# Kernel tuning notes

Hardware: AMD Instinct MI355X
Metric: run time of the kernel (lower is better)

## Reference

```python
import jax, jax.numpy as jnp
import numpy as np

GRID_SIZE = 5
SPLINE_ORDER = 3
FP_DIM = 2513        # mixed fingerprint: MACCS + PubChem + ErG + Morgan
FP_2_DIM = 512
HIDDEN_DIM = 300
BATCH = 8192


def make_grid(in_features):
    # Matches KANLinear buffer: arange(-so, gs+so+1)*h + grid_range[0], expanded per feature
    h = 2.0 / GRID_SIZE  # (grid_range[1]-grid_range[0]) / grid_size with range [-1, 1]
    g = jnp.arange(-SPLINE_ORDER, GRID_SIZE + SPLINE_ORDER + 1, dtype=jnp.float32) * h - 1.0
    return jnp.broadcast_to(g[None, :], (in_features, g.shape[0]))  # [in, 12]


def b_splines(x, grid):
    # x: [B, in] -> bases: [B, in, grid_size + spline_order]
    x = x[:, :, None]  # [B, in, 1]
    bases = ((x >= grid[:, :-1]) & (x < grid[:, 1:])).astype(x.dtype)
    for k in range(1, SPLINE_ORDER + 1):
        bases = ((x - grid[:, :-(k + 1)]) / (grid[:, k:-1] - grid[:, :-(k + 1)]) * bases[..., :-1]
                 + (grid[:, k + 1:] - x) / (grid[:, k + 1:] - grid[:, 1:-k]) * bases[..., 1:])
    return bases  # [B, in, K]


def kan_linear(x, base_w, spline_w, scaler):
    # base path: SiLU(x) @ base_w.T
    base_out = jax.nn.silu(x) @ base_w.T  # [B, out]
    # spline path: flatten bases and scaled spline weights into one GEMM
    in_f = x.shape[1]
    grid = make_grid(in_f)
    bs = b_splines(x, grid).reshape(x.shape[0], -1)               # [B, in*K]
    sw = (spline_w * scaler[:, :, None]).reshape(spline_w.shape[0], -1)  # [out, in*K]
    return base_out + bs @ sw.T


def setup_inputs() -> dict:
    key = jax.random.key(0)
    ks = jax.random.split(key, 8)
    K = GRID_SIZE + SPLINE_ORDER
    def kaiming(k, shape, fan_in):
        bound = 1.0 / np.sqrt(fan_in)
        return jax.random.uniform(k, shape, jnp.float32, -bound, bound)
    return {
        "fp": jax.random.uniform(ks[0], (BATCH, FP_DIM), jnp.float32),
        "base_w1": kaiming(ks[1], (FP_2_DIM, FP_DIM), FP_DIM),
        "spline_w1": jax.random.normal(ks[2], (FP_2_DIM, FP_DIM, K), jnp.float32) * 0.02,
        "scaler1": kaiming(ks[3], (FP_2_DIM, FP_DIM), FP_DIM),
        "base_w2": kaiming(ks[4], (HIDDEN_DIM, FP_2_DIM), FP_2_DIM),
        "spline_w2": jax.random.normal(ks[5], (HIDDEN_DIM, FP_2_DIM, K), jnp.float32) * 0.02,
        "scaler2": kaiming(ks[6], (HIDDEN_DIM, FP_2_DIM), FP_2_DIM),
    }


def reference(fp, base_w1, spline_w1, scaler1, base_w2, spline_w2, scaler2):
    # FPN forward (eval mode, dropout=identity): fc1 (KAN) -> ReLU -> fc2 (KAN)
    h = kan_linear(fp, base_w1, spline_w1, scaler1)   # [B, fp_2_dim]
    h = jax.nn.relu(h)
    out = kan_linear(h, base_w2, spline_w2, scaler2)  # [B, hidden]
    return out
```

## Files before the change

### kernel.cpp

```cpp
#include <hip/hip_runtime.h>
#include <stdint.h>

typedef unsigned short ushort_t;
typedef __attribute__((ext_vector_type(8))) __bf16 bf16x8;
typedef __attribute__((ext_vector_type(4))) float f32x4;
typedef __attribute__((ext_vector_type(4))) uint32_t u32x4;
typedef __attribute__((ext_vector_type(4))) float float4_t;

#define GPTR(x) ((__attribute__((address_space(1))) void*)(x))
#define LPTR(x) ((__attribute__((address_space(3))) void*)(x))

#define M8   8192
#define KT   5888
#define NKT  184
#define LDW1 17664
#define O1   512
#define K2   3584
#define NK2  112
#define O2P  384

__device__ __forceinline__ ushort_t f2b(float f) {
  union { float f; uint32_t i; } v; v.f = f;
  uint32_t x = v.i;
  uint32_t r = (x + 0x7FFFu + ((x >> 16) & 1u)) >> 16;
  return (ushort_t)r;
}

__device__ __forceinline__ void spline_expand(float x, float* sil, float* b ) {
  *sil = x / (1.0f + __expf(-x));
  float g[12];
#pragma unroll
  for (int j = 0; j < 12; ++j) g[j] = (float)(j - 3) * 0.4f - 1.0f;
  float t[11];
#pragma unroll
  for (int j = 0; j < 11; ++j) t[j] = (x >= g[j] && x < g[j + 1]) ? 1.0f : 0.0f;
#pragma unroll
  for (int k = 1; k <= 3; ++k) {
#pragma unroll
    for (int j = 0; j + k < 11; ++j) {
      float i1 = 1.0f / (g[j + k] - g[j]);
      float i2 = 1.0f / (g[j + k + 1] - g[j + 1]);
      t[j] = (x - g[j]) * i1 * t[j] + (g[j + k + 1] - x) * i2 * t[j + 1];
    }
  }
#pragma unroll
  for (int k = 0; k < 8; ++k) b[k] = t[k];
}

__global__ __launch_bounds__(256) void expand_third(
    const float* __restrict__ xin, ushort_t* __restrict__ A1t, int f0, int fcnt) {
  __shared__ __align__(16) ushort_t sb[KT];
  const int row = blockIdx.x, tid = threadIdx.x;
  for (int t = tid; t < (KT >> 1); t += 256) ((uint32_t*)sb)[t] = 0;
  __syncthreads();
  const float* xr = xin + (size_t)row * 2513 + f0;
#pragma unroll
  for (int j = 0; j < 1024; j += 256) {
    int fl = j + tid;
    if (fl < fcnt) {
      float sil, b[8];
      spline_expand(xr[fl], &sil, b);
      ushort_t* o = &sb[fl * 7];
      o[0] = f2b(sil);
#pragma unroll
      for (int k = 0; k < 6; ++k) o[1 + k] = f2b(b[2 + k]);
    }
  }
  __syncthreads();
  u32x4* dst = (u32x4*)(A1t + (size_t)row * KT);
  const u32x4* src = (const u32x4*)sb;
  for (int t = tid; t < (KT >> 3); t += 256) dst[t] = src[t];
}

__global__ __launch_bounds__(256) void prepw_all(
    const float* __restrict__ bw1, const float* __restrict__ sw1, const float* __restrict__ sc1,
    const float* __restrict__ bw2, const float* __restrict__ sw2, const float* __restrict__ sc2,
    ushort_t* __restrict__ W1, ushort_t* __restrict__ W2) {
  __shared__ __align__(16) ushort_t sb[KT];
  const int bx = blockIdx.x, c = blockIdx.y, tid = threadIdx.x;
  const float *bw, *sw, *sc;
  ushort_t* dst;
  int in_f, o, out_f, ce, f0, fcnt;
  if (bx < 512) {
    o = bx; out_f = 512; in_f = 2513;
    ce = KT; f0 = c * 838;
    fcnt = (c == 2) ? 837 : 838;
    dst = W1 + (size_t)o * LDW1 + c * KT;
    bw = bw1; sw = sw1; sc = sc1;
  } else {
    if (c > 0) return;
    o = bx - 512; out_f = 300; in_f = 512;
    ce = K2; f0 = 0; fcnt = 512;
    dst = W2 + (size_t)o * K2;
    bw = bw2; sw = sw2; sc = sc2;
  }
  for (int t = tid; t < (ce >> 1); t += 256) ((uint32_t*)sb)[t] = 0;
  __syncthreads();
  if (o < out_f) {
#pragma unroll
    for (int j = 0; j < 1024; j += 256) {
      int fl = j + tid;
      if (fl < fcnt) {
        size_t base = (size_t)o * in_f + f0 + fl;
        float s = sc[base];
        float4_t s0 = ((const float4_t*)(sw + base * 8))[0];
        float4_t s1 = ((const float4_t*)(sw + base * 8))[1];
        ushort_t* w = &sb[fl * 7];
        w[0] = f2b(bw[base]);
        w[1] = f2b(s0.z * s); w[2] = f2b(s0.w * s);
        w[3] = f2b(s1.x * s); w[4] = f2b(s1.y * s);
        w[5] = f2b(s1.z * s); w[6] = f2b(s1.w * s);
      }
    }
  }
  __syncthreads();
  u32x4* d4 = (u32x4*)dst;
  const u32x4* s4 = (const u32x4*)sb;
  for (int t = tid; t < (ce >> 3); t += 256) d4[t] = s4[t];
}


__global__ __launch_bounds__(256) void gemm1_kernel(
    const ushort_t* __restrict__ A, const ushort_t* __restrict__ Bw,
    float* __restrict__ P, int accum) {
  __shared__ __align__(16) ushort_t As[2][128 * 32];
  __shared__ __align__(16) ushort_t Bs[2][128 * 32];
  const int tid = threadIdx.x;
  const int m0 = blockIdx.x * 128;
  const int n0 = blockIdx.y * 128;
  const int s = blockIdx.z;
  const int k0 = s * 61;
  const int k1 = (s == 2) ? NKT : (k0 + 61);
  const int lane = tid & 63;
  const int wv = tid >> 6;
  const int wm = wv & 1, wn = wv >> 1;
  const int l15 = lane & 15, lq = lane >> 4;
  const int rxor = (l15 >> 2) & 1;
  const int csw = ((lq ^ (l15 & 3)) << 3);

  f32x4 acc[4][4];
#pragma unroll
  for (int a = 0; a < 4; ++a)
#pragma unroll
    for (int b = 0; b < 4; ++b) acc[a][b] = {0.0f, 0.0f, 0.0f, 0.0f};

  const int u0 = tid, u1 = tid + 256;
  const int r0 = u0 >> 2, c0 = u0 & 3;
  const int r1 = u1 >> 2, c1 = u1 & 3;
  const int lr0 = r0 ^ ((r0 >> 2) & 1), lc0 = c0 ^ (lr0 & 3);
  const int lr1 = r1 ^ ((r1 >> 2) & 1), lc1 = c1 ^ (lr1 & 3);
  const ushort_t* gA0 = A + (size_t)(m0 + lr0) * KT + lc0 * 8;
  const ushort_t* gA1 = A + (size_t)(m0 + lr1) * KT + lc1 * 8;
  const ushort_t* gB0 = Bw + (size_t)(n0 + lr0) * LDW1 + lc0 * 8;
  const ushort_t* gB1 = Bw + (size_t)(n0 + lr1) * LDW1 + lc1 * 8;

#define STG1(bb, kk) do { const int kb_ = (kk) << 5; \
    __builtin_amdgcn_global_load_lds(GPTR(gA0 + kb_), LPTR(&As[bb][u0 * 8]), 16, 0, 0); \
    __builtin_amdgcn_global_load_lds(GPTR(gA1 + kb_), LPTR(&As[bb][u1 * 8]), 16, 0, 0); \
    __builtin_amdgcn_global_load_lds(GPTR(gB0 + kb_), LPTR(&Bs[bb][u0 * 8]), 16, 0, 0); \
    __builtin_amdgcn_global_load_lds(GPTR(gB1 + kb_), LPTR(&Bs[bb][u1 * 8]), 16, 0, 0); \
  } while (0)

  STG1(0, k0);
  __syncthreads();
  const int nst = k1 - k0;
  for (int i = 0; i < nst; ++i) {
    const int cur = i & 1;
    if (i + 1 < nst) STG1(cur ^ 1, k0 + i + 1);
    bf16x8 aF[4], bF[4];
#pragma unroll
    for (int t = 0; t < 4; ++t) {
      const int ar = ((wm * 64 + t * 16 + l15) ^ rxor) * 32 + csw;
      const int br = ((wn * 64 + t * 16 + l15) ^ rxor) * 32 + csw;
      aF[t] = *(const bf16x8*)(&As[cur][ar]);
      bF[t] = *(const bf16x8*)(&Bs[cur][br]);
    }
#pragma unroll
    for (int ti = 0; ti < 4; ++ti)
#pragma unroll
      for (int tj = 0; tj < 4; ++tj)
        acc[ti][tj] = __builtin_amdgcn_mfma_f32_16x16x32_bf16(aF[ti], bF[tj], acc[ti][tj], 0, 0, 0);
    __syncthreads();
  }
#undef STG1

  float* Pp = P + (size_t)s * M8 * O1;
#pragma unroll
  for (int ti = 0; ti < 4; ++ti) {
#pragma unroll
    for (int tj = 0; tj < 4; ++tj) {
      int gr = m0 + wm * 64 + ti * 16 + lq * 4;
      int gc = n0 + wn * 64 + tj * 16 + l15;
#pragma unroll
      for (int rr = 0; rr < 4; ++rr) {
        size_t pi = (size_t)(gr + rr) * O1 + gc;
        float v = acc[ti][tj][rr];
        if (accum) v += Pp[pi];
        Pp[pi] = v;
      }
    }
  }
}

__global__ __launch_bounds__(256) void reduce_expand_stage(
    const float* __restrict__ P, ushort_t* __restrict__ A2) {
  __shared__ __align__(16) ushort_t sb[K2];
  const int row = blockIdx.x, tid = threadIdx.x;
  const size_t total = (size_t)M8 * O1;
#pragma unroll
  for (int j = 0; j < 512; j += 256) {
    int f = j + tid;
    size_t idx = (size_t)row * O1 + f;
    float v = P[idx] + P[total + idx] + P[2 * total + idx];
    if (v < 0.0f) v = 0.0f;
    float sil, b[8];
    spline_expand(v, &sil, b);
    ushort_t* o = &sb[f * 7];
    o[0] = f2b(sil);
#pragma unroll
    for (int k = 0; k < 6; ++k) o[1 + k] = f2b(b[2 + k]);
  }
  __syncthreads();
  u32x4* dst = (u32x4*)(A2 + (size_t)row * K2);
  const u32x4* src = (const u32x4*)sb;
  for (int t = tid; t < (K2 >> 3); t += 256) dst[t] = src[t];
}

__global__ __launch_bounds__(256) void gemm2_kernel(
    const ushort_t* __restrict__ A, const ushort_t* __restrict__ Bw,
    float* __restrict__ P2) {
  __shared__ __align__(16) ushort_t As[2][64 * 32];
  __shared__ __align__(16) ushort_t Bs[2][128 * 32];
  const int tid = threadIdx.x;
  const int m0 = blockIdx.x * 64;
  const int n0 = blockIdx.y * 128;
  const int s = blockIdx.z;
  const int k0 = s * 56, k1 = k0 + 56;
  const int lane = tid & 63;
  const int wv = tid >> 6;
  const int wm = wv & 1, wn = wv >> 1;
  const int l15 = lane & 15, lq = lane >> 4;
  const int rxor = (l15 >> 2) & 1;
  const int csw = ((lq ^ (l15 & 3)) << 3);

  f32x4 acc[2][4];
#pragma unroll
  for (int a = 0; a < 2; ++a)
#pragma unroll
    for (int b = 0; b < 4; ++b) acc[a][b] = {0.0f, 0.0f, 0.0f, 0.0f};

  const int uA = tid;
  const int rA = uA >> 2, cA = uA & 3;
  const int lrA = rA ^ ((rA >> 2) & 1), lcA = cA ^ (lrA & 3);
  const int u0 = tid, u1 = tid + 256;
  const int rB0 = u0 >> 2, cB0 = u0 & 3;
  const int rB1 = u1 >> 2, cB1 = u1 & 3;
  const int lrB0 = rB0 ^ ((rB0 >> 2) & 1), lcB0 = cB0 ^ (lrB0 & 3);
  const int lrB1 = rB1 ^ ((rB1 >> 2) & 1), lcB1 = cB1 ^ (lrB1 & 3);
  const ushort_t* gA  = A + (size_t)(m0 + lrA) * K2 + lcA * 8;
  const ushort_t* gB0 = Bw + (size_t)(n0 + lrB0) * K2 + lcB0 * 8;
  const ushort_t* gB1 = Bw + (size_t)(n0 + lrB1) * K2 + lcB1 * 8;

#define STG2(bb, kk) do { const int kb_ = (kk) << 5; \
    __builtin_amdgcn_global_load_lds(GPTR(gA + kb_),  LPTR(&As[bb][uA * 8]), 16, 0, 0); \
    __builtin_amdgcn_global_load_lds(GPTR(gB0 + kb_), LPTR(&Bs[bb][u0 * 8]), 16, 0, 0); \
    __builtin_amdgcn_global_load_lds(GPTR(gB1 + kb_), LPTR(&Bs[bb][u1 * 8]), 16, 0, 0); \
  } while (0)

  STG2(0, k0);
  __syncthreads();
  const int nst = k1 - k0;
  for (int i = 0; i < nst; ++i) {
    const int cur = i & 1;
    if (i + 1 < nst) STG2(cur ^ 1, k0 + i + 1);
    bf16x8 aF[2], bF[4];
#pragma unroll
    for (int t = 0; t < 2; ++t) {
      const int ar = ((wm * 32 + t * 16 + l15) ^ rxor) * 32 + csw;
      aF[t] = *(const bf16x8*)(&As[cur][ar]);
    }
#pragma unroll
    for (int t = 0; t < 4; ++t) {
      const int br = ((wn * 64 + t * 16 + l15) ^ rxor) * 32 + csw;
      bF[t] = *(const bf16x8*)(&Bs[cur][br]);
    }
#pragma unroll
    for (int ti = 0; ti < 2; ++ti)
#pragma unroll
      for (int tj = 0; tj < 4; ++tj)
        acc[ti][tj] = __builtin_amdgcn_mfma_f32_16x16x32_bf16(aF[ti], bF[tj], acc[ti][tj], 0, 0, 0);
    __syncthreads();
  }
#undef STG2

  float* Pp = P2 + (size_t)s * M8 * O2P;
#pragma unroll
  for (int ti = 0; ti < 2; ++ti) {
#pragma unroll
    for (int tj = 0; tj < 4; ++tj) {
      int gr = m0 + wm * 32 + ti * 16 + lq * 4;
      int gc = n0 + wn * 64 + tj * 16 + l15;
#pragma unroll
      for (int rr = 0; rr < 4; ++rr)
        Pp[(size_t)(gr + rr) * O2P + gc] = acc[ti][tj][rr];
    }
  }
}

__global__ void reduce_out_kernel(const float* __restrict__ P2, float* __restrict__ out) {
  int idx = blockIdx.x * 256 + threadIdx.x;
  const int total = M8 * O2P;
  if (idx >= total) return;
  float v = P2[idx] + P2[(size_t)total + idx];
  int r = idx / O2P, c = idx - r * O2P;
  if (c < 300) out[(size_t)r * 300 + c] = v;
}

static inline size_t alup(size_t x) { return (x + 255) & ~(size_t)255; }

extern "C" void kernel_launch(void* const* d_in, const int* in_sizes, int n_in,
                              void* d_out, int out_size, void* d_ws, size_t ws_size,
                              hipStream_t stream) {
  const float* fp  = (const float*)d_in[0];
  const float* bw1 = (const float*)d_in[1];
  const float* sw1 = (const float*)d_in[2];
  const float* sc1 = (const float*)d_in[3];
  const float* bw2 = (const float*)d_in[4];
  const float* sw2 = (const float*)d_in[5];
  const float* sc2 = (const float*)d_in[6];
  float* out = (float*)d_out;

  char* wp = (char*)d_ws;
  size_t off = 0;
  ushort_t* W1a = (ushort_t*)(wp + off); off += alup((size_t)O1 * LDW1 * 2);
  ushort_t* W2a = (ushort_t*)(wp + off); off += alup((size_t)O2P * K2 * 2);
  float*    P   = (float*)(wp + off);    off += alup((size_t)3 * M8 * O1 * 4);
  ushort_t* A2c = (ushort_t*)(wp + off); off += alup((size_t)M8 * K2 * 2);
  ushort_t* A1t = (ushort_t*)(wp + off); off += alup((size_t)M8 * KT * 2);

  prepw_all<<<dim3(896, 3), 256, 0, stream>>>(bw1, sw1, sc1, bw2, sw2, sc2, W1a, W2a);

  for (int p = 0; p < 3; ++p) {
    const int f0 = p * 838;
    const int fcnt = (p == 2) ? 837 : 838;
    expand_third<<<M8, 256, 0, stream>>>(fp, A1t, f0, fcnt);
    gemm1_kernel<<<dim3(M8 / 128, O1 / 128, 3), 256, 0, stream>>>(A1t, W1a + p * KT, P, p > 0 ? 1 : 0);
  }

  reduce_expand_stage<<<M8, 256, 0, stream>>>(P, A2c);
  gemm2_kernel<<<dim3(M8 / 64, 3, 2), 256, 0, stream>>>(A2c, W2a, P);
  reduce_out_kernel<<<(M8 * O2P + 255) / 256, 256, 0, stream>>>(P, out);

  (void)in_sizes; (void)n_in; (void)out_size; (void)ws_size;
}
```

Baseline: 579.6 us.

## Triple-buffer LDS in both GEMMs with explicit vmcnt waits for deeper prefetch

Both GEMM kernels move from double to triple-buffered LDS staging. Two K-tiles are prefetched ahead, and each iteration waits on a partial vmcnt count instead of draining all outstanding loads. This lets global-to-LDS loads for tile i+2 overlap with MFMA work on tile i, hiding memory latency. The cost is 50% more LDS per block, which may reduce occupancy, and a dependence on exact vmcnt counts and on no other outstanding loads.

After: 576.1 us. Within noise of the previous version (-0.6%).

```diff
diff --git a/kernel.cpp b/kernel.cpp
--- a/kernel.cpp
+++ b/kernel.cpp
@@ -123,8 +123,8 @@
 __global__ __launch_bounds__(256) void gemm1_kernel(
     const ushort_t* __restrict__ A, const ushort_t* __restrict__ Bw,
     float* __restrict__ P, int accum) {
-  __shared__ __align__(16) ushort_t As[2][128 * 32];
-  __shared__ __align__(16) ushort_t Bs[2][128 * 32];
+  __shared__ __align__(16) ushort_t As[3][128 * 32];
+  __shared__ __align__(16) ushort_t Bs[3][128 * 32];
   const int tid = threadIdx.x;
   const int m0 = blockIdx.x * 128;
   const int n0 = blockIdx.y * 128;
@@ -161,28 +161,48 @@
     __builtin_amdgcn_global_load_lds(GPTR(gB1 + kb_), LPTR(&Bs[bb][u1 * 8]), 16, 0, 0); \
   } while (0)
 
+#define COMP1(bb) do { \
+    bf16x8 aF[4], bF[4]; \
+    _Pragma("unroll") \
+    for (int t = 0; t < 4; ++t) { \
+      const int ar = ((wm * 64 + t * 16 + l15) ^ rxor) * 32 + csw; \
+      const int br = ((wn * 64 + t * 16 + l15) ^ rxor) * 32 + csw; \
+      aF[t] = *(const bf16x8*)(&As[bb][ar]); \
+      bF[t] = *(const bf16x8*)(&Bs[bb][br]); \
+    } \
+    _Pragma("unroll") \
+    for (int ti = 0; ti < 4; ++ti) \
+      _Pragma("unroll") \
+      for (int tj = 0; tj < 4; ++tj) \
+        acc[ti][tj] = __builtin_amdgcn_mfma_f32_16x16x32_bf16(aF[ti], bF[tj], acc[ti][tj], 0, 0, 0); \
+  } while (0)
+
+  const int nst = k1 - k0;
   STG1(0, k0);
-  __syncthreads();
-  const int nst = k1 - k0;
-  for (int i = 0; i < nst; ++i) {
-    const int cur = i & 1;
-    if (i + 1 < nst) STG1(cur ^ 1, k0 + i + 1);
-    bf16x8 aF[4], bF[4];
-#pragma unroll
-    for (int t = 0; t < 4; ++t) {
-      const int ar = ((wm * 64 + t * 16 + l15) ^ rxor) * 32 + csw;
-      const int br = ((wn * 64 + t * 16 + l15) ^ rxor) * 32 + csw;
-      aF[t] = *(const bf16x8*)(&As[cur][ar]);
-      bF[t] = *(const bf16x8*)(&Bs[cur][br]);
-    }
-#pragma unroll
-    for (int ti = 0; ti < 4; ++ti)
-#pragma unroll
-      for (int tj = 0; tj < 4; ++tj)
-        acc[ti][tj] = __builtin_amdgcn_mfma_f32_16x16x32_bf16(aF[ti], bF[tj], acc[ti][tj], 0, 0, 0);
-    __syncthreads();
-  }
+  STG1(1, k0 + 1);
+  int b0 = 0, b1 = 1, b2 = 2;
+  for (int i = 0; i < nst - 2; ++i) {
+    STG1(b2, k0 + i + 2);
+    asm volatile("s_waitcnt vmcnt(8)" ::: "memory");
+    __builtin_amdgcn_s_barrier();
+    __builtin_amdgcn_sched_barrier(0);
+    COMP1(b0);
+    __builtin_amdgcn_sched_barrier(0);
+    __builtin_amdgcn_s_barrier();
+    int tswp = b0; b0 = b1; b1 = b2; b2 = tswp;
+  }
+  asm volatile("s_waitcnt vmcnt(4)" ::: "memory");
+  __builtin_amdgcn_s_barrier();
+  __builtin_amdgcn_sched_barrier(0);
+  COMP1(b0);
+  __builtin_amdgcn_sched_barrier(0);
+  __builtin_amdgcn_s_barrier();
+  asm volatile("s_waitcnt vmcnt(0)" ::: "memory");
+  __builtin_amdgcn_s_barrier();
+  __builtin_amdgcn_sched_barrier(0);
+  COMP1(b1);
 #undef STG1
+#undef COMP1
 
   float* Pp = P + (size_t)s * M8 * O1;
 #pragma unroll
@@ -229,13 +249,13 @@
 __global__ __launch_bounds__(256) void gemm2_kernel(
     const ushort_t* __restrict__ A, const ushort_t* __restrict__ Bw,
     float* __restrict__ P2) {
-  __shared__ __align__(16) ushort_t As[2][64 * 32];
-  __shared__ __align__(16) ushort_t Bs[2][128 * 32];
+  __shared__ __align__(16) ushort_t As[3][64 * 32];
+  __shared__ __align__(16) ushort_t Bs[3][128 * 32];
   const int tid = threadIdx.x;
   const int m0 = blockIdx.x * 64;
   const int n0 = blockIdx.y * 128;
   const int s = blockIdx.z;
-  const int k0 = s * 56, k1 = k0 + 56;
+  const int k0 = s * 56;
   const int lane = tid & 63;
   const int wv = tid >> 6;
   const int wm = wv & 1, wn = wv >> 1;
@@ -267,31 +287,51 @@
     __builtin_amdgcn_global_load_lds(GPTR(gB1 + kb_), LPTR(&Bs[bb][u1 * 8]), 16, 0, 0); \
   } while (0)
 
+#define COMP2(bb) do { \
+    bf16x8 aF[2], bF[4]; \
+    _Pragma("unroll") \
+    for (int t = 0; t < 2; ++t) { \
+      const int ar = ((wm * 32 + t * 16 + l15) ^ rxor) * 32 + csw; \
+      aF[t] = *(const bf16x8*)(&As[bb][ar]); \
+    } \
+    _Pragma("unroll") \
+    for (int t = 0; t < 4; ++t) { \
+      const int br = ((wn * 64 + t * 16 + l15) ^ rxor) * 32 + csw; \
+      bF[t] = *(const bf16x8*)(&Bs[bb][br]); \
+    } \
+    _Pragma("unroll") \
+    for (int ti = 0; ti < 2; ++ti) \
+      _Pragma("unroll") \
+      for (int tj = 0; tj < 4; ++tj) \
+        acc[ti][tj] = __builtin_amdgcn_mfma_f32_16x16x32_bf16(aF[ti], bF[tj], acc[ti][tj], 0, 0, 0); \
+  } while (0)
+
+  const int nst = 56;
   STG2(0, k0);
-  __syncthreads();
-  const int nst = k1 - k0;
-  for (int i = 0; i < nst; ++i) {
-    const int cur = i & 1;
-    if (i + 1 < nst) STG2(cur ^ 1, k0 + i + 1);
-    bf16x8 aF[2], bF[4];
-#pragma unroll
-    for (int t = 0; t < 2; ++t) {
-      const int ar = ((wm * 32 + t * 16 + l15) ^ rxor) * 32 + csw;
-      aF[t] = *(const bf16x8*)(&As[cur][ar]);
-    }
-#pragma unroll
-    for (int t = 0; t < 4; ++t) {
-      const int br = ((wn * 64 + t * 16 + l15) ^ rxor) * 32 + csw;
-      bF[t] = *(const bf16x8*)(&Bs[cur][br]);
-    }
-#pragma unroll
-    for (int ti = 0; ti < 2; ++ti)
-#pragma unroll
-      for (int tj = 0; tj < 4; ++tj)
-        acc[ti][tj] = __builtin_amdgcn_mfma_f32_16x16x32_bf16(aF[ti], bF[tj], acc[ti][tj], 0, 0, 0);
-    __syncthreads();
-  }
+  STG2(1, k0 + 1);
+  int b0 = 0, b1 = 1, b2 = 2;
+  for (int i = 0; i < nst - 2; ++i) {
+    STG2(b2, k0 + i + 2);
+    asm volatile("s_waitcnt vmcnt(6)" ::: "memory");
+    __builtin_amdgcn_s_barrier();
+    __builtin_amdgcn_sched_barrier(0);
+    COMP2(b0);
+    __builtin_amdgcn_sched_barrier(0);
+    __builtin_amdgcn_s_barrier();
+    int tswp = b0; b0 = b1; b1 = b2; b2 = tswp;
+  }
+  asm volatile("s_waitcnt vmcnt(3)" ::: "memory");
+  __builtin_amdgcn_s_barrier();
+  __builtin_amdgcn_sched_barrier(0);
+  COMP2(b0);
+  __builtin_amdgcn_sched_barrier(0);
+  __builtin_amdgcn_s_barrier();
+  asm volatile("s_waitcnt vmcnt(0)" ::: "memory");
+  __builtin_amdgcn_s_barrier();
+  __builtin_amdgcn_sched_barrier(0);
+  COMP2(b1);
 #undef STG2
+#undef COMP2
 
   float* Pp = P2 + (size_t)s * M8 * O2P;
 #pragma unroll
```

## Fuse spline expansion of layer-1 inputs into the GEMM A-tile producer

Applied to the files above, without the earlier changes.

Removes the three expand_third passes and their bf16 A1t round trip through global memory. The layer-1 GEMM now reads raw fp values, computes the SiLU and the six non-zero B-spline bases in registers, and writes them into the LDS A tile while the next B tile streams in. Each feature is padded to 8 bf16 slots (K=20128) in a single K pass with a 4-way split-K, which drops the accumulate read-modify-write passes over P. In exchange every N-block recomputes the spline expansion, there is ~14% more padded K work, and an extra partial buffer has to be reduced.

Measured after the change: 731.4 us. +26.2%, slower.

```diff
diff --git a/kernel.cpp b/kernel.cpp
--- a/kernel.cpp
+++ b/kernel.cpp
@@ -11,12 +11,10 @@
 #define LPTR(x) ((__attribute__((address_space(3))) void*)(x))
 
 #define M8   8192
-#define KT   5888
-#define NKT  184
-#define LDW1 17664
+#define K1P  20128
+#define NK1  629
 #define O1   512
 #define K2   3584
-#define NK2  112
 #define O2P  384
 
 __device__ __forceinline__ ushort_t f2b(float f) {
@@ -26,111 +24,105 @@
   return (ushort_t)r;
 }
 
-__device__ __forceinline__ void spline_expand(float x, float* sil, float* b ) {
+__device__ __forceinline__ void spline7(float x, float* sil, float* b6) {
   *sil = x / (1.0f + __expf(-x));
   float g[12];
 #pragma unroll
   for (int j = 0; j < 12; ++j) g[j] = (float)(j - 3) * 0.4f - 1.0f;
   float t[11];
 #pragma unroll
-  for (int j = 0; j < 11; ++j) t[j] = (x >= g[j] && x < g[j + 1]) ? 1.0f : 0.0f;
+  for (int j = 2; j < 11; ++j) t[j] = (x >= g[j] && x < g[j + 1]) ? 1.0f : 0.0f;
 #pragma unroll
   for (int k = 1; k <= 3; ++k) {
 #pragma unroll
-    for (int j = 0; j + k < 11; ++j) {
+    for (int j = 2; j + k < 11; ++j) {
       float i1 = 1.0f / (g[j + k] - g[j]);
       float i2 = 1.0f / (g[j + k + 1] - g[j + 1]);
       t[j] = (x - g[j]) * i1 * t[j] + (g[j + k + 1] - x) * i2 * t[j + 1];
     }
   }
 #pragma unroll
-  for (int k = 0; k < 8; ++k) b[k] = t[k];
-}
-
-__global__ __launch_bounds__(256) void expand_third(
-    const float* __restrict__ xin, ushort_t* __restrict__ A1t, int f0, int fcnt) {
-  __shared__ __align__(16) ushort_t sb[KT];
-  const int row = blockIdx.x, tid = threadIdx.x;
-  for (int t = tid; t < (KT >> 1); t += 256) ((uint32_t*)sb)[t] = 0;
-  __syncthreads();
-  const float* xr = xin + (size_t)row * 2513 + f0;
-#pragma unroll
-  for (int j = 0; j < 1024; j += 256) {
-    int fl = j + tid;
-    if (fl < fcnt) {
-      float sil, b[8];
-      spline_expand(xr[fl], &sil, b);
-      ushort_t* o = &sb[fl * 7];
-      o[0] = f2b(sil);
-#pragma unroll
-      for (int k = 0; k < 6; ++k) o[1 + k] = f2b(b[2 + k]);
-    }
-  }
-  __syncthreads();
-  u32x4* dst = (u32x4*)(A1t + (size_t)row * KT);
-  const u32x4* src = (const u32x4*)sb;
-  for (int t = tid; t < (KT >> 3); t += 256) dst[t] = src[t];
+  for (int k = 0; k < 6; ++k) b6[k] = t[2 + k];
+}
+
+__device__ __forceinline__ void expand_pack_write(ushort_t* dst, float x, bool ok) {
+  float sil, b6[6];
+  spline7(x, &sil, b6);
+  u32x4 wv;
+  wv[0] = (uint32_t)f2b(sil)   | ((uint32_t)f2b(b6[0]) << 16);
+  wv[1] = (uint32_t)f2b(b6[1]) | ((uint32_t)f2b(b6[2]) << 16);
+  wv[2] = (uint32_t)f2b(b6[3]) | ((uint32_t)f2b(b6[4]) << 16);
+  wv[3] = (uint32_t)f2b(b6[5]);
+  if (!ok) { wv[0] = 0; wv[1] = 0; wv[2] = 0; wv[3] = 0; }
+  *(u32x4*)dst = wv;
 }
 
 __global__ __launch_bounds__(256) void prepw_all(
     const float* __restrict__ bw1, const float* __restrict__ sw1, const float* __restrict__ sc1,
     const float* __restrict__ bw2, const float* __restrict__ sw2, const float* __restrict__ sc2,
     ushort_t* __restrict__ W1, ushort_t* __restrict__ W2) {
-  __shared__ __align__(16) ushort_t sb[KT];
-  const int bx = blockIdx.x, c = blockIdx.y, tid = threadIdx.x;
-  const float *bw, *sw, *sc;
-  ushort_t* dst;
-  int in_f, o, out_f, ce, f0, fcnt;
+  __shared__ __align__(16) ushort_t sb[K1P];
+  const int bx = blockIdx.x, tid = threadIdx.x;
   if (bx < 512) {
-    o = bx; out_f = 512; in_f = 2513;
-    ce = KT; f0 = c * 838;
-    fcnt = (c == 2) ? 837 : 838;
-    dst = W1 + (size_t)o * LDW1 + c * KT;
-    bw = bw1; sw = sw1; sc = sc1;
-  } else {
-    if (c > 0) return;
-    o = bx - 512; out_f = 300; in_f = 512;
-    ce = K2; f0 = 0; fcnt = 512;
-    dst = W2 + (size_t)o * K2;
-    bw = bw2; sw = sw2; sc = sc2;
-  }
-  for (int t = tid; t < (ce >> 1); t += 256) ((uint32_t*)sb)[t] = 0;
-  __syncthreads();
-  if (o < out_f) {
-#pragma unroll
-    for (int j = 0; j < 1024; j += 256) {
+    const int o = bx;
+    for (int t = tid; t < (K1P >> 1); t += 256) ((uint32_t*)sb)[t] = 0;
+    __syncthreads();
+#pragma unroll
+    for (int j = 0; j < 2560; j += 256) {
       int fl = j + tid;
-      if (fl < fcnt) {
-        size_t base = (size_t)o * in_f + f0 + fl;
-        float s = sc[base];
-        float4_t s0 = ((const float4_t*)(sw + base * 8))[0];
-        float4_t s1 = ((const float4_t*)(sw + base * 8))[1];
-        ushort_t* w = &sb[fl * 7];
-        w[0] = f2b(bw[base]);
+      if (fl < 2513) {
+        size_t base = (size_t)o * 2513 + fl;
+        float s = sc1[base];
+        float4_t s0 = ((const float4_t*)(sw1 + base * 8))[0];
+        float4_t s1 = ((const float4_t*)(sw1 + base * 8))[1];
+        ushort_t* w = &sb[fl * 8];
+        w[0] = f2b(bw1[base]);
         w[1] = f2b(s0.z * s); w[2] = f2b(s0.w * s);
         w[3] = f2b(s1.x * s); w[4] = f2b(s1.y * s);
         w[5] = f2b(s1.z * s); w[6] = f2b(s1.w * s);
       }
     }
-  }
-  __syncthreads();
-  u32x4* d4 = (u32x4*)dst;
-  const u32x4* s4 = (const u32x4*)sb;
-  for (int t = tid; t < (ce >> 3); t += 256) d4[t] = s4[t];
-}
-
-
-__global__ __launch_bounds__(256) void gemm1_kernel(
-    const ushort_t* __restrict__ A, const ushort_t* __restrict__ Bw,
-    float* __restrict__ P, int accum) {
+    __syncthreads();
+    u32x4* d4 = (u32x4*)(W1 + (size_t)o * K1P);
+    const u32x4* s4 = (const u32x4*)sb;
+    for (int t = tid; t < (K1P >> 3); t += 256) d4[t] = s4[t];
+  } else {
+    const int o = bx - 512;
+    for (int t = tid; t < (K2 >> 1); t += 256) ((uint32_t*)sb)[t] = 0;
+    __syncthreads();
+    if (o < 300) {
+#pragma unroll
+      for (int j = 0; j < 512; j += 256) {
+        int fl = j + tid;
+        size_t base = (size_t)o * 512 + fl;
+        float s = sc2[base];
+        float4_t s0 = ((const float4_t*)(sw2 + base * 8))[0];
+        float4_t s1 = ((const float4_t*)(sw2 + base * 8))[1];
+        ushort_t* w = &sb[fl * 7];
+        w[0] = f2b(bw2[base]);
+        w[1] = f2b(s0.z * s); w[2] = f2b(s0.w * s);
+        w[3] = f2b(s1.x * s); w[4] = f2b(s1.y * s);
+        w[5] = f2b(s1.z * s); w[6] = f2b(s1.w * s);
+      }
+    }
+    __syncthreads();
+    u32x4* d4 = (u32x4*)(W2 + (size_t)o * K2);
+    const u32x4* s4 = (const u32x4*)sb;
+    for (int t = tid; t < (K2 >> 3); t += 256) d4[t] = s4[t];
+  }
+}
+
+__global__ __launch_bounds__(256) void gemm1_fused(
+    const float* __restrict__ X, const ushort_t* __restrict__ Bw,
+    float* __restrict__ P) {
   __shared__ __align__(16) ushort_t As[2][128 * 32];
   __shared__ __align__(16) ushort_t Bs[2][128 * 32];
   const int tid = threadIdx.x;
   const int m0 = blockIdx.x * 128;
   const int n0 = blockIdx.y * 128;
   const int s = blockIdx.z;
-  const int k0 = s * 61;
-  const int k1 = (s == 2) ? NKT : (k0 + 61);
+  const int k0 = s * 157;
+  const int k1 = (s == 3) ? NK1 : (k0 + 157);
   const int lane = tid & 63;
   const int wv = tid >> 6;
   const int wm = wv & 1, wn = wv >> 1;
@@ -144,45 +136,68 @@
 #pragma unroll
     for (int b = 0; b < 4; ++b) acc[a][b] = {0.0f, 0.0f, 0.0f, 0.0f};
 
-  const int u0 = tid, u1 = tid + 256;
-  const int r0 = u0 >> 2, c0 = u0 & 3;
-  const int r1 = u1 >> 2, c1 = u1 & 3;
+  const int r0 = tid >> 2, c0 = tid & 3;
+  const int r1 = r0 + 64,  c1 = c0;
   const int lr0 = r0 ^ ((r0 >> 2) & 1), lc0 = c0 ^ (lr0 & 3);
   const int lr1 = r1 ^ ((r1 >> 2) & 1), lc1 = c1 ^ (lr1 & 3);
-  const ushort_t* gA0 = A + (size_t)(m0 + lr0) * KT + lc0 * 8;
-  const ushort_t* gA1 = A + (size_t)(m0 + lr1) * KT + lc1 * 8;
-  const ushort_t* gB0 = Bw + (size_t)(n0 + lr0) * LDW1 + lc0 * 8;
-  const ushort_t* gB1 = Bw + (size_t)(n0 + lr1) * LDW1 + lc1 * 8;
-
-#define STG1(bb, kk) do { const int kb_ = (kk) << 5; \
-    __builtin_amdgcn_global_load_lds(GPTR(gA0 + kb_), LPTR(&As[bb][u0 * 8]), 16, 0, 0); \
-    __builtin_amdgcn_global_load_lds(GPTR(gA1 + kb_), LPTR(&As[bb][u1 * 8]), 16, 0, 0); \
-    __builtin_amdgcn_global_load_lds(GPTR(gB0 + kb_), LPTR(&Bs[bb][u0 * 8]), 16, 0, 0); \
-    __builtin_amdgcn_global_load_lds(GPTR(gB1 + kb_), LPTR(&Bs[bb][u1 * 8]), 16, 0, 0); \
+  const float* xr0 = X + (size_t)(m0 + lr0) * 2513;
+  const float* xr1 = X + (size_t)(m0 + lr1) * 2513;
+  const ushort_t* gB0 = Bw + (size_t)(n0 + lr0) * K1P + lc0 * 8;
+  const ushort_t* gB1 = Bw + (size_t)(n0 + lr1) * K1P + lc1 * 8;
+
+#define STGB(bb, kk) do { const int kb_ = (kk) << 5; \
+    __builtin_amdgcn_global_load_lds(GPTR(gB0 + kb_), LPTR(&Bs[bb][tid * 8]), 16, 0, 0); \
+    __builtin_amdgcn_global_load_lds(GPTR(gB1 + kb_), LPTR(&Bs[bb][(tid + 256) * 8]), 16, 0, 0); \
   } while (0)
 
-  STG1(0, k0);
+#define COMP1(bb) do { \
+    bf16x8 aF[4], bF[4]; \
+    _Pragma("unroll") \
+    for (int t = 0; t < 4; ++t) { \
+      const int ar = ((wm * 64 + t * 16 + l15) ^ rxor) * 32 + csw; \
+      const int br = ((wn * 64 + t * 16 + l15) ^ rxor) * 32 + csw; \
+      aF[t] = *(const bf16x8*)(&As[bb][ar]); \
+      bF[t] = *(const bf16x8*)(&Bs[bb][br]); \
+    } \
+    _Pragma("unroll") \
+    for (int ti = 0; ti < 4; ++ti) \
+      _Pragma("unroll") \
+      for (int tj = 0; tj < 4; ++tj) \
+        acc[ti][tj] = __builtin_amdgcn_mfma_f32_16x16x32_bf16(aF[ti], bF[tj], acc[ti][tj], 0, 0, 0); \
+  } while (0)
+
+  {
+    int f0 = k0 * 4 + lc0, f1 = k0 * 4 + lc1;
+    bool ok0 = f0 < 2513, ok1 = f1 < 2513;
+    float xv0 = ok0 ? xr0[f0] : 0.0f;
+    float xv1 = ok1 ? xr1[f1] : 0.0f;
+    STGB(0, k0);
+    expand_pack_write(&As[0][tid * 8], xv0, ok0);
+    expand_pack_write(&As[0][(tid + 256) * 8], xv1, ok1);
+  }
   __syncthreads();
   const int nst = k1 - k0;
   for (int i = 0; i < nst; ++i) {
     const int cur = i & 1;
-    if (i + 1 < nst) STG1(cur ^ 1, k0 + i + 1);
-    bf16x8 aF[4], bF[4];
-#pragma unroll
-    for (int t = 0; t < 4; ++t) {
-      const int ar = ((wm * 64 + t * 16 + l15) ^ rxor) * 32 + csw;
-      const int br = ((wn * 64 + t * 16 + l15) ^ rxor) * 32 + csw;
-      aF[t] = *(const bf16x8*)(&As[cur][ar]);
-      bF[t] = *(const bf16x8*)(&Bs[cur][br]);
-    }
-#pragma unroll
-    for (int ti = 0; ti < 4; ++ti)
-#pragma unroll
-      for (int tj = 0; tj < 4; ++tj)
-        acc[ti][tj] = __builtin_amdgcn_mfma_f32_16x16x32_bf16(aF[ti], bF[tj], acc[ti][tj], 0, 0, 0);
-    __syncthreads();
-  }
-#undef STG1
+    float nx0 = 0.0f, nx1 = 0.0f;
+    bool nok0 = false, nok1 = false;
+    if (i + 1 < nst) {
+      const int kk = k0 + i + 1;
+      const int nf0 = kk * 4 + lc0, nf1 = kk * 4 + lc1;
+      nok0 = nf0 < 2513; nok1 = nf1 < 2513;
+      nx0 = nok0 ? xr0[nf0] : 0.0f;
+      nx1 = nok1 ? xr1[nf1] : 0.0f;
+      STGB(cur ^ 1, kk);
+    }
+    COMP1(cur);
+    if (i + 1 < nst) {
+      expand_pack_write(&As[cur ^ 1][tid * 8], nx0, nok0);
+      expand_pack_write(&As[cur ^ 1][(tid + 256) * 8], nx1, nok1);
+    }
+    __syncthreads();
+  }
+#undef STGB
+#undef COMP1
 
   float* Pp = P + (size_t)s * M8 * O1;
 #pragma unroll
@@ -192,12 +207,8 @@
       int gr = m0 + wm * 64 + ti * 16 + lq * 4;
       int gc = n0 + wn * 64 + tj * 16 + l15;
 #pragma unroll
-      for (int rr = 0; rr < 4; ++rr) {
-        size_t pi = (size_t)(gr + rr) * O1 + gc;
-        float v = acc[ti][tj][rr];
-        if (accum) v += Pp[pi];
-        Pp[pi] = v;
-      }
+      for (int rr = 0; rr < 4; ++rr)
+        Pp[(size_t)(gr + rr) * O1 + gc] = acc[ti][tj][rr];
     }
   }
 }
@@ -211,14 +222,14 @@
   for (int j = 0; j < 512; j += 256) {
     int f = j + tid;
     size_t idx = (size_t)row * O1 + f;
-    float v = P[idx] + P[total + idx] + P[2 * total + idx];
+    float v = P[idx] + P[total + idx] + P[2 * total + idx] + P[3 * total + idx];
     if (v < 0.0f) v = 0.0f;
-    float sil, b[8];
-    spline_expand(v, &sil, b);
+    float sil, b6[6];
+    spline7(v, &sil, b6);
     ushort_t* o = &sb[f * 7];
     o[0] = f2b(sil);
 #pragma unroll
-    for (int k = 0; k < 6; ++k) o[1 + k] = f2b(b[2 + k]);
+    for (int k = 0; k < 6; ++k) o[1 + k] = f2b(b6[k]);
   }
   __syncthreads();
   u32x4* dst = (u32x4*)(A2 + (size_t)row * K2);
@@ -332,20 +343,14 @@
 
   char* wp = (char*)d_ws;
   size_t off = 0;
-  ushort_t* W1a = (ushort_t*)(wp + off); off += alup((size_t)O1 * LDW1 * 2);
+  ushort_t* W1a = (ushort_t*)(wp + off); off += alup((size_t)O1 * K1P * 2);
   ushort_t* W2a = (ushort_t*)(wp + off); off += alup((size_t)O2P * K2 * 2);
-  float*    P   = (float*)(wp + off);    off += alup((size_t)3 * M8 * O1 * 4);
+  float*    P   = (float*)(wp + off);    off += alup((size_t)4 * M8 * O1 * 4);
   ushort_t* A2c = (ushort_t*)(wp + off); off += alup((size_t)M8 * K2 * 2);
-  ushort_t* A1t = (ushort_t*)(wp + off); off += alup((size_t)M8 * KT * 2);
-
-  prepw_all<<<dim3(896, 3), 256, 0, stream>>>(bw1, sw1, sc1, bw2, sw2, sc2, W1a, W2a);
-
-  for (int p = 0; p < 3; ++p) {
-    const int f0 = p * 838;
-    const int fcnt = (p == 2) ? 837 : 838;
-    expand_third<<<M8, 256, 0, stream>>>(fp, A1t, f0, fcnt);
-    gemm1_kernel<<<dim3(M8 / 128, O1 / 128, 3), 256, 0, stream>>>(A1t, W1a + p * KT, P, p > 0 ? 1 : 0);
-  }
+
+  prepw_all<<<dim3(896), 256, 0, stream>>>(bw1, sw1, sc1, bw2, sw2, sc2, W1a, W2a);
+
+  gemm1_fused<<<dim3(M8 / 128, O1 / 128, 4), 256, 0, stream>>>(fp, W1a, P);
 
   reduce_expand_stage<<<M8, 256, 0, stream>>>(P, A2c);
   gemm2_kernel<<<dim3(M8 / 64, 3, 2), 256, 0, stream>>>(A2c, W2a, P);
```
